# Kernel optimization log

Measured on AMD Instinct MI355X. Metric: run time of the kernel, lower is better.

The kernel has to match this reference:

```python
import jax, jax.numpy as jnp
import numpy as np


def _gcn_conv(x, W, b, row, col, norm, n_nodes):
    # x: [N, Fin]; W: [Fin, Fout]. PyG GCNConv: linear -> normalized gather/scatter-add -> +bias
    h = x @ W                                   # [N, Fout]
    msgs = h[row] * norm[:, None]               # [E+N, Fout] gather + scale
    out = jax.ops.segment_sum(msgs, col, num_segments=n_nodes)  # scatter-add
    return out + b


def _gcn_norm(edge_index, n_nodes):
    # add self-loops, then sym-normalize: deg^{-1/2}[row] * deg^{-1/2}[col]
    loops = jnp.arange(n_nodes, dtype=edge_index.dtype)
    row = jnp.concatenate([edge_index[0], loops])
    col = jnp.concatenate([edge_index[1], loops])
    ones = jnp.ones(row.shape[0], dtype=jnp.float32)
    deg = jax.ops.segment_sum(ones, col, num_segments=n_nodes)
    dinv = jnp.where(deg > 0, jax.lax.rsqrt(deg), 0.0)
    norm = dinv[row] * dinv[col]
    return row, col, norm


def setup_inputs() -> dict:
    key = jax.random.key(0)
    k1, k2, k3, k4 = jax.random.split(key, 4)
    N, E, F, H, C = 100000, 1600000, 256, 128, 40
    x = jax.random.normal(k1, (N, F), dtype=jnp.float32)
    edge_index = jax.random.randint(k2, (2, E), 0, N, dtype=jnp.int64)
    W1 = jax.random.normal(k3, (F, H), dtype=jnp.float32) * (1.0 / np.sqrt(F))
    b1 = jnp.zeros((H,), dtype=jnp.float32)
    W2 = jax.random.normal(k4, (H, C), dtype=jnp.float32) * (1.0 / np.sqrt(H))
    b2 = jnp.zeros((C,), dtype=jnp.float32)
    return {"x": x, "edge_index": edge_index, "W1": W1, "b1": b1, "W2": W2, "b2": b2}


def reference(x, edge_index, W1, b1, W2, b2):
    n_nodes = x.shape[0]
    row, col, norm = _gcn_norm(edge_index, n_nodes)
    h = _gcn_conv(x, W1, b1, row, col, norm, n_nodes)
    h = jax.nn.relu(h)
    # F.dropout in eval mode is identity (reference run deterministically)
    h = _gcn_conv(h, W2, b2, row, col, norm, n_nodes)
    return jax.nn.log_softmax(h, axis=1)
```

## Files before the change

### kernel.cpp

```cpp
#include <hip/hip_runtime.h>
#include <hip/hip_bf16.h>
#include <math.h>
#include <stdint.h>

typedef unsigned short u16;
typedef unsigned int u32;
typedef __attribute__((ext_vector_type(8))) short short8;
typedef __attribute__((ext_vector_type(4))) float f32x4;
typedef __attribute__((ext_vector_type(2))) float f32x2;

#define BN 256
#define NBMAX 400
#define EPB 4096
#define ST1 160
#define ST2 192

__device__ __forceinline__ u16 bfbits(float f) {
    __hip_bfloat16 h = __float2bfloat16(f);
    return *reinterpret_cast<u16*>(&h);
}
__device__ __forceinline__ float bflo(u32 v) { return __uint_as_float(v << 16); }
__device__ __forceinline__ float bfhi(u32 v) { return __uint_as_float(v & 0xffff0000u); }

template <bool HI>
__device__ __forceinline__ f32x2 fp8pair(u32 v) {
#if __has_builtin(__builtin_amdgcn_cvt_pk_f32_fp8)
    return __builtin_amdgcn_cvt_pk_f32_fp8(v, HI);
#else
    f32x2 r;
    r.x = __builtin_amdgcn_cvt_f32_fp8(v, HI ? 2 : 0);
    r.y = __builtin_amdgcn_cvt_f32_fp8(v, HI ? 3 : 1);
    return r;
#endif
}

__device__ __forceinline__ int sigma128(int col) {
    int a = col >> 6, c = (col >> 4) & 3, lr = col & 15;
    return (a << 6) + (lr << 2) + c;
}

__global__ __launch_bounds__(256) void k_pre(const int* __restrict__ ei, int E, int n, int nb,
                                             int nblkc, int* __restrict__ gcnt,
                                             const float* __restrict__ w1, short* __restrict__ w1bf,
                                             const float* __restrict__ b1, const float* __restrict__ w2,
                                             float* __restrict__ b1p, float* __restrict__ w2p) {
    __shared__ int sh[NBMAX];
    const int t = threadIdx.x;
    const int b = blockIdx.x;
    if (b < nblkc) {
        const int* col = ei + E;
        for (int i = t; i < nb; i += 256) sh[i] = 0;
        __syncthreads();
        const int base = b * EPB;
#pragma unroll
        for (int j = 0; j < 16; ++j) {
            int e = base + j * 256 + t;
            if (e < E) {
                unsigned c = (unsigned)col[e];
                if (c < (unsigned)n) atomicAdd(&sh[c >> 8], 1);
            }
        }
        __syncthreads();
        for (int i = t; i < nb; i += 256)
            if (sh[i]) atomicAdd(&gcnt[i], sh[i]);
    } else if (b < nblkc + 128) {
        int i = (b - nblkc) * 256 + t;
        int e = i & 7, l = (i >> 3) & 63, kt = (i >> 9) & 7, ct = i >> 12;
        int k = kt * 32 + (l >> 4) * 8 + e;
        int c = ct * 16 + (l & 15);
        w1bf[i] = (short)bfbits(w1[(size_t)k * 128 + c]);
    } else {
        int i = (b - nblkc - 128) * 256 + t;
        if (i < 128) b1p[sigma128(i)] = b1[i];
        int j = i - 128;
        if (j >= 0 && j < 128 * 40) {
            int col = j / 40, jj = j - col * 40;
            w2p[sigma128(col) * 40 + jj] = w2[j];
        }
    }
}

__global__ __launch_bounds__(512) void k_bscan(const int* __restrict__ gcnt,
                                               int* __restrict__ ebase, int* __restrict__ cursor,
                                               int* __restrict__ off, int nb, int n) {
    __shared__ int sh[512];
    const int t = threadIdx.x;
    int v = (t < nb) ? gcnt[t] : 0;
    sh[t] = v;
    __syncthreads();
    for (int d = 1; d < 512; d <<= 1) {
        int x = (t >= d) ? sh[t - d] : 0;
        __syncthreads();
        sh[t] += x;
        __syncthreads();
    }
    if (t < nb) {
        int excl = sh[t] - v;
        ebase[t] = excl;
        cursor[t] = excl;
    }
    if (t == 0) {
        ebase[nb] = sh[511];
        off[n] = sh[511] + n;
    }
}

__global__ __launch_bounds__(256) void k_scatg1(const int* __restrict__ ei,
                                                int* __restrict__ cursor, u32* __restrict__ staging,
                                                int E, int n, int nb, int nblks,
                                                const float* __restrict__ x,
                                                const short* __restrict__ w1bf,
                                                u32* __restrict__ hbf8) {
    __shared__ int cnt[NBMAX];
    __shared__ int cbase[NBMAX];
    const int t = threadIdx.x;
    if ((int)blockIdx.x < nblks) {
        for (int i = t; i < nb; i += 256) cnt[i] = 0;
        __syncthreads();
        const int base = blockIdx.x * EPB;
        int rr[16], cc[16], rk[16];
#pragma unroll
        for (int j = 0; j < 16; ++j) {
            int e = base + j * 256 + t;
            cc[j] = -1;
            if (e < E) {
                unsigned r = (unsigned)ei[e], c = (unsigned)ei[E + e];
                if (r < (unsigned)n && c < (unsigned)n) {
                    rr[j] = (int)r;
                    cc[j] = (int)c;
                    rk[j] = atomicAdd(&cnt[c >> 8], 1);
                }
            }
        }
        __syncthreads();
        for (int i = t; i < nb; i += 256)
            if (cnt[i]) cbase[i] = atomicAdd(&cursor[i], cnt[i]);
        __syncthreads();
#pragma unroll
        for (int j = 0; j < 16; ++j) {
            if (cc[j] >= 0) {
                int b = cc[j] >> 8;
                staging[cbase[b] + rk[j]] = (u32)rr[j] | ((u32)(cc[j] & (BN - 1)) << 17);
            }
        }
        return;
    }
    const int bid = blockIdx.x - nblks;
    const int wv = t >> 6, l = t & 63;
    const int mrow = wv >> 1, mcol = wv & 1;
    const int lr = l & 15, kg = l >> 4;
    const int n0 = bid * 64;

    const float* xp[2];
#pragma unroll
    for (int m = 0; m < 2; ++m) {
        int row = n0 + 32 * mrow + 16 * m + lr;
        if (row > n - 1) row = n - 1;
        xp[m] = x + (size_t)row * 256 + kg * 8;
    }
    const short* bbase = w1bf + ((size_t)(4 * mcol) * 8) * 64 * 8 + (size_t)l * 8;

    float4 xv[2][8][2];
#pragma unroll
    for (int kt = 0; kt < 8; ++kt)
#pragma unroll
        for (int m = 0; m < 2; ++m) {
            xv[m][kt][0] = *(const float4*)(xp[m] + kt * 32);
            xv[m][kt][1] = *(const float4*)(xp[m] + kt * 32 + 4);
        }

    f32x4 zero = {0.f, 0.f, 0.f, 0.f};
    f32x4 acc[2][4];
#pragma unroll
    for (int m = 0; m < 2; ++m)
#pragma unroll
        for (int c = 0; c < 4; ++c) acc[m][c] = zero;

#pragma unroll
    for (int kt = 0; kt < 8; ++kt) {
        short8 af[2];
#pragma unroll
        for (int m = 0; m < 2; ++m) {
            float4 u = xv[m][kt][0];
            float4 v = xv[m][kt][1];
            short8 a;
            a[0] = (short)bfbits(u.x);
            a[1] = (short)bfbits(u.y);
            a[2] = (short)bfbits(u.z);
            a[3] = (short)bfbits(u.w);
            a[4] = (short)bfbits(v.x);
            a[5] = (short)bfbits(v.y);
            a[6] = (short)bfbits(v.z);
            a[7] = (short)bfbits(v.w);
            af[m] = a;
        }
#pragma unroll
        for (int c = 0; c < 4; ++c) {
            short8 bfrag = *(const short8*)(bbase + ((size_t)(c * 8 + kt) * 64) * 8);
#pragma unroll
            for (int m = 0; m < 2; ++m)
                acc[m][c] = __builtin_amdgcn_mfma_f32_16x16x32_bf16(af[m], bfrag,
                                                                    acc[m][c], 0, 0, 0);
        }
    }

#pragma unroll
    for (int m = 0; m < 2; ++m) {
        int rbase = n0 + 32 * mrow + 16 * m + kg * 4;
#pragma unroll
        for (int r = 0; r < 4; ++r) {
            int row = rbase + r;
            if (row < n) {
                int w = __builtin_amdgcn_cvt_pk_fp8_f32(acc[m][0][r], acc[m][1][r], 0, false);
                w = __builtin_amdgcn_cvt_pk_fp8_f32(acc[m][2][r], acc[m][3][r], w, true);
                hbf8[(size_t)row * 32 + 16 * mcol + lr] = (u32)w;
            }
        }
    }
}

__global__ __launch_bounds__(256) void k_build(const u32* __restrict__ staging,
                                               const int* __restrict__ ebase,
                                               int* __restrict__ csrs, int* __restrict__ off,
                                               float* __restrict__ dinv, int n) {
    __shared__ int sh[256];
    __shared__ int cur[256];
    const int t = threadIdx.x;
    const int b = blockIdx.x;
    const int e0 = ebase[b], e1 = ebase[b + 1];
    const int node0 = b * BN;
    const int nn = min(BN, n - node0);
    sh[t] = 0;
    __syncthreads();
    for (int i = e0 + t; i < e1; i += 256)
        atomicAdd(&sh[staging[i] >> 17], 1);
    __syncthreads();
    const int mycnt = sh[t];
    const int myval = (t < nn) ? mycnt + 1 : 0;
    sh[t] = myval;
    __syncthreads();
    for (int d = 1; d < 256; d <<= 1) {
        int x = (t >= d) ? sh[t - d] : 0;
        __syncthreads();
        sh[t] += x;
        __syncthreads();
    }
    const int excl = sh[t] - myval;
    const int csrbase = e0 + node0;
    if (t < nn) {
        int node = node0 + t;
        int o = csrbase + excl;
        off[node] = o;
        dinv[node] = rsqrtf((float)(mycnt + 1));
        csrs[o] = node;
        cur[t] = o + 1;
    }
    __syncthreads();
    for (int i = e0 + t; i < e1; i += 256) {
        u32 v = staging[i];
        int p = atomicAdd(&cur[v >> 17], 1);
        csrs[p] = (int)(v & 0x1FFFF);
    }
}

__global__ __launch_bounds__(256) void k_agg1(const u32* __restrict__ hbf8,
                                              const int* __restrict__ off,
                                              const int* __restrict__ csrs,
                                              const float* __restrict__ dinv,
                                              const float* __restrict__ b1p,
                                              u16* __restrict__ h1b, int n) {
    __shared__ int s_s[8][ST1];
    __shared__ float s_f[8][ST1];
    const int t = threadIdx.x, h = t >> 5, fl = t & 31;
    const int node = blockIdx.x * 8 + h;
    const int nd = node < n ? node : n - 1;
    const float dn = dinv[nd];
    const int e0 = off[nd], e1 = off[nd + 1];
    const int deg = e1 - e0;
    const int nst = deg < ST1 ? deg : ST1;
    for (int i = fl; i < nst; i += 32) {
        int s = csrs[e0 + i];
        s_s[h][i] = s;
        s_f[h][i] = dinv[s] * dn;
    }
    __syncthreads();

    const int onst = __shfl_xor(nst, 32, 64);
    const int nmin = nst < onst ? nst : onst;
    const int nmax = nst > onst ? nst : onst;
    const int odeg = __shfl_xor(deg, 32, 64);
    const int dmax = deg > odeg ? deg : odeg;

    const u32* hb = hbf8;
    float a0 = 0.f, a1 = 0.f, a2 = 0.f, a3 = 0.f;
    int i = 0;
    for (; i + 16 <= nmin; i += 16) {
        u32 vv[16];
        float ww[16];
#pragma unroll
        for (int k = 0; k < 16; ++k) {
            int s = s_s[h][i + k];
            ww[k] = s_f[h][i + k];
            vv[k] = hb[(size_t)s * 32 + fl];
        }
#pragma unroll
        for (int k = 0; k < 16; ++k) {
            f32x2 lo = fp8pair<false>(vv[k]), hi = fp8pair<true>(vv[k]);
            a0 = fmaf(lo.x, ww[k], a0); a1 = fmaf(lo.y, ww[k], a1);
            a2 = fmaf(hi.x, ww[k], a2); a3 = fmaf(hi.y, ww[k], a3);
        }
    }
    for (; i + 4 <= nmin; i += 4) {
        u32 vv[4];
        float ww[4];
#pragma unroll
        for (int k = 0; k < 4; ++k) {
            int s = s_s[h][i + k];
            ww[k] = s_f[h][i + k];
            vv[k] = hb[(size_t)s * 32 + fl];
        }
#pragma unroll
        for (int k = 0; k < 4; ++k) {
            f32x2 lo = fp8pair<false>(vv[k]), hi = fp8pair<true>(vv[k]);
            a0 = fmaf(lo.x, ww[k], a0); a1 = fmaf(lo.y, ww[k], a1);
            a2 = fmaf(hi.x, ww[k], a2); a3 = fmaf(hi.y, ww[k], a3);
        }
    }
    for (; i < nmin; ++i) {
        int s = s_s[h][i];
        float w = s_f[h][i];
        u32 v = hb[(size_t)s * 32 + fl];
        f32x2 lo = fp8pair<false>(v), hi = fp8pair<true>(v);
        a0 = fmaf(lo.x, w, a0); a1 = fmaf(lo.y, w, a1);
        a2 = fmaf(hi.x, w, a2); a3 = fmaf(hi.y, w, a3);
    }
    for (; i < nmax; ++i) {
        bool ok = i < nst;
        int s = ok ? s_s[h][i] : nd;
        float w = ok ? s_f[h][i] : 0.f;
        u32 v = hb[(size_t)s * 32 + fl];
        f32x2 lo = fp8pair<false>(v), hi = fp8pair<true>(v);
        a0 = fmaf(lo.x, w, a0); a1 = fmaf(lo.y, w, a1);
        a2 = fmaf(hi.x, w, a2); a3 = fmaf(hi.y, w, a3);
    }
    for (int j = ST1; j < dmax; ++j) {
        bool ok = j < deg;
        int s = ok ? csrs[e0 + j] : nd;
        float w = ok ? dinv[s] * dn : 0.f;
        u32 v = hb[(size_t)s * 32 + fl];
        f32x2 lo = fp8pair<false>(v), hi = fp8pair<true>(v);
        a0 = fmaf(lo.x, w, a0); a1 = fmaf(lo.y, w, a1);
        a2 = fmaf(hi.x, w, a2); a3 = fmaf(hi.y, w, a3);
    }

    float4 bb = *(const float4*)(b1p + 4 * fl);
    float r0 = fmaxf(a0 + bb.x, 0.f);
    float r1 = fmaxf(a1 + bb.y, 0.f);
    float r2 = fmaxf(a2 + bb.z, 0.f);
    float r3 = fmaxf(a3 + bb.w, 0.f);
    if (node < n) {
        uint2 o;
        o.x = (u32)bfbits(r0) | ((u32)bfbits(r1) << 16);
        o.y = (u32)bfbits(r2) | ((u32)bfbits(r3) << 16);
        ((uint2*)h1b)[(size_t)node * 32 + fl] = o;
    }
}

__global__ __launch_bounds__(64) void k_gemm2(const u16* __restrict__ h1b,
                                              const float* __restrict__ w2p,
                                              u32* __restrict__ h2q, float* __restrict__ scl,
                                              int n) {
    __shared__ float hs[64 * 132];
    const int t = threadIdx.x;
    const int n0 = blockIdx.x * 64;
    const uint4* src = (const uint4*)(h1b + (size_t)n0 * 128);
#pragma unroll
    for (int i = 0; i < 16; ++i) {
        int idx = i * 64 + t;
        int r = idx >> 4, q = idx & 15;
        uint4 v = make_uint4(0u, 0u, 0u, 0u);
        if (n0 + r < n) v = src[(size_t)r * 16 + q];
        *(float4*)&hs[r * 132 + q * 8] =
            make_float4(bflo(v.x), bfhi(v.x), bflo(v.y), bfhi(v.y));
        *(float4*)&hs[r * 132 + q * 8 + 4] =
            make_float4(bflo(v.z), bfhi(v.z), bflo(v.w), bfhi(v.w));
    }
    __syncthreads();

    float acc[40];
#pragma unroll
    for (int c = 0; c < 40; ++c) acc[c] = 0.f;

    for (int k4 = 0; k4 < 32; ++k4) {
        float4 hv = *(const float4*)&hs[t * 132 + 4 * k4];
#pragma unroll
        for (int j = 0; j < 4; ++j) {
            float xv = (j == 0) ? hv.x : (j == 1) ? hv.y : (j == 2) ? hv.z : hv.w;
            const float* wr = w2p + (size_t)(4 * k4 + j) * 40;
#pragma unroll
            for (int c = 0; c < 40; ++c) acc[c] = fmaf(xv, wr[c], acc[c]);
        }
    }
    __syncthreads();

    float mx = 0.f;
#pragma unroll
    for (int c = 0; c < 40; ++c) mx = fmaxf(mx, fabsf(acc[c]));
    const float qs = mx > 0.f ? 127.f / mx : 0.f;
    u32* rowp = (u32*)hs + t * 16;
#pragma unroll
    for (int j = 0; j < 10; ++j) {
        u32 w = 0;
#pragma unroll
        for (int k = 0; k < 4; ++k) {
            int q = __float2int_rn(acc[4 * j + k] * qs);
            q = q > 127 ? 127 : (q < -127 ? -127 : q);
            w |= ((u32)(q & 255)) << (8 * k);
        }
        rowp[j] = w;
    }
#pragma unroll
    for (int j = 10; j < 16; ++j) rowp[j] = 0;
    __syncthreads();
    const int nrow = (n - n0 < 64) ? n - n0 : 64;
    uint4* dst = (uint4*)(h2q + (size_t)n0 * 16);
    const uint4* s4 = (const uint4*)hs;
#pragma unroll
    for (int i = 0; i < 4; ++i) {
        int idx = i * 64 + t;
        if ((idx >> 2) < nrow) dst[idx] = s4[idx];
    }
    if (t < nrow) scl[n0 + t] = mx * (1.f / 127.f);
}

__global__ __launch_bounds__(256) void k_agg2(const u32* __restrict__ h2q,
                                              const float* __restrict__ scl,
                                              const int* __restrict__ off,
                                              const int* __restrict__ csrs,
                                              const float* __restrict__ dinv,
                                              const float* __restrict__ b2,
                                              float* __restrict__ out, int n) {
    __shared__ int s_s[4][ST2];
    __shared__ float s_f[4][ST2];
    const int t = threadIdx.x, wv = t >> 6, l = t & 63;
    const int node = blockIdx.x * 4 + wv;
    const int nd = node < n ? node : n - 1;
    const float dn = dinv[nd];
    const int e0 = off[nd], e1 = off[nd + 1];
    const int deg = e1 - e0;
    const int nst = deg < ST2 ? deg : ST2;
    for (int i = l; i < nst; i += 64) {
        int s = csrs[e0 + i];
        s_s[wv][i] = s;
        s_f[wv][i] = dinv[s] * dn * scl[s];
    }
    __syncthreads();

    const int g = l >> 4;
    const int fl = l & 15;

#define ACC4(v, w)                                                         \
    {                                                                      \
        a0 = fmaf((float)(int)(signed char)((v) & 0xff), (w), a0);         \
        a1 = fmaf((float)(int)(signed char)(((v) >> 8) & 0xff), (w), a1);  \
        a2 = fmaf((float)(int)(signed char)(((v) >> 16) & 0xff), (w), a2); \
        a3 = fmaf((float)(int)(signed char)((v) >> 24), (w), a3);          \
    }

    float a0 = 0.f, a1 = 0.f, a2 = 0.f, a3 = 0.f;
    int base = 0;
    for (; base + 16 <= nst; base += 16) {
        int eA = base + g, eB = base + 4 + g, eC = base + 8 + g, eD = base + 12 + g;
        int sA = s_s[wv][eA], sB = s_s[wv][eB], sC = s_s[wv][eC], sD = s_s[wv][eD];
        float wA = s_f[wv][eA], wB = s_f[wv][eB], wC = s_f[wv][eC], wD = s_f[wv][eD];
        u32 vA = h2q[(size_t)sA * 16 + fl];
        u32 vB = h2q[(size_t)sB * 16 + fl];
        u32 vC = h2q[(size_t)sC * 16 + fl];
        u32 vD = h2q[(size_t)sD * 16 + fl];
        ACC4(vA, wA); ACC4(vB, wB); ACC4(vC, wC); ACC4(vD, wD);
    }
    for (; base < nst; base += 4) {
        int e = base + g;
        bool ok = e < nst;
        int s = ok ? s_s[wv][e] : nd;
        float w = ok ? s_f[wv][e] : 0.f;
        u32 v = h2q[(size_t)s * 16 + fl];
        ACC4(v, w);
    }
    for (int j = nst; j < deg; j += 4) {
        int e = j + g;
        bool ok = e < deg;
        int s = ok ? csrs[e0 + e] : nd;
        float w = ok ? dinv[s] * dn * scl[s] : 0.f;
        u32 v = h2q[(size_t)s * 16 + fl];
        ACC4(v, w);
    }
#undef ACC4

    float t0 = __shfl(a0, (l + 32) & 63, 64);
    float t1 = __shfl(a1, (l + 32) & 63, 64);
    float t2 = __shfl(a2, (l + 32) & 63, 64);
    float t3 = __shfl(a3, (l + 32) & 63, 64);
    a0 += t0; a1 += t1; a2 += t2; a3 += t3;
    t0 = __shfl(a0, (l + 16) & 63, 64);
    t1 = __shfl(a1, (l + 16) & 63, 64);
    t2 = __shfl(a2, (l + 16) & 63, 64);
    t3 = __shfl(a3, (l + 16) & 63, 64);
    a0 += t0; a1 += t1; a2 += t2; a3 += t3;

    const bool act = (l < 10);
    float4 bb = *(const float4*)(b2 + 4 * (act ? l : 9));
    float v0 = a0 + bb.x, v1 = a1 + bb.y, v2 = a2 + bb.z, v3 = a3 + bb.w;

    float m = act ? fmaxf(fmaxf(v0, v1), fmaxf(v2, v3)) : -INFINITY;
#pragma unroll
    for (int d = 8; d > 0; d >>= 1) m = fmaxf(m, __shfl_xor(m, d, 16));
    float s = act ? (__expf(v0 - m) + __expf(v1 - m) + __expf(v2 - m) + __expf(v3 - m)) : 0.f;
#pragma unroll
    for (int d = 8; d > 0; d >>= 1) s += __shfl_xor(s, d, 16);
    float ls = logf(s);
    if (node < n && act) {
        float4 o = make_float4(v0 - m - ls, v1 - m - ls, v2 - m - ls, v3 - m - ls);
        *(float4*)(out + (size_t)node * 40 + 4 * l) = o;
    }
}

extern "C" void kernel_launch(void* const* d_in, const int* in_sizes, int n_in,
                              void* d_out, int out_size, void* d_ws, size_t ws_size,
                              hipStream_t stream) {
    const float* x = (const float*)d_in[0];
    const int* ei = (const int*)d_in[1];
    const float* w1 = (const float*)d_in[2];
    const float* b1 = (const float*)d_in[3];
    const float* w2 = (const float*)d_in[4];
    const float* b2 = (const float*)d_in[5];
    float* out = (float*)d_out;

    const int N = in_sizes[0] / 256;
    const int E = in_sizes[1] / 2;
    const int NB = (N + BN - 1) / BN;

    char* p = (char*)d_ws;
    auto alloc = [&](size_t bytes) {
        char* r = p;
        p += (bytes + 255) & ~(size_t)255;
        return r;
    };
    int* gcnt = (int*)alloc((size_t)NB * 4);
    int* ebase = (int*)alloc((size_t)(NB + 1) * 4);
    int* cursor = (int*)alloc((size_t)NB * 4);
    int* off = (int*)alloc((size_t)(N + 1) * 4);
    float* dinv = (float*)alloc((size_t)N * 4);
    float* scl = (float*)alloc((size_t)N * 4);
    int* csrs = (int*)alloc((size_t)(E + N) * 4);
    short* w1bf = (short*)alloc(32768 * 2);
    float* b1p = (float*)alloc(128 * 4);
    float* w2p = (float*)alloc(128 * 40 * 4);
    u32* hbf8 = (u32*)alloc((size_t)N * 32 * 4);
    u16* h1b = (u16*)alloc((size_t)N * 128 * 2);
    u32* staging = (u32*)h1b;
    u32* h2q = hbf8;

    const int nblk = (E + EPB - 1) / EPB;
    const int g1blk = (N + 63) / 64;

    (void)hipMemsetAsync(gcnt, 0, (size_t)NB * 4, stream);
    k_pre<<<nblk + 128 + 21, 256, 0, stream>>>(ei, E, N, NB, nblk, gcnt, w1, w1bf,
                                               b1, w2, b1p, w2p);
    k_bscan<<<1, 512, 0, stream>>>(gcnt, ebase, cursor, off, NB, N);
    k_scatg1<<<nblk + g1blk, 256, 0, stream>>>(ei, cursor, staging, E, N, NB, nblk,
                                               x, w1bf, hbf8);
    k_build<<<NB, 256, 0, stream>>>(staging, ebase, csrs, off, dinv, N);
    k_agg1<<<(N + 7) / 8, 256, 0, stream>>>(hbf8, off, csrs, dinv, b1p, h1b, N);
    k_gemm2<<<g1blk, 64, 0, stream>>>(h1b, w2p, h2q, scl, N);
    k_agg2<<<(N + 3) / 4, 256, 0, stream>>>(h2q, scl, off, csrs, dinv, b2, out, N);
}
```

Baseline: 244.4 us.

## Stage x tile through swizzled LDS as bf16 before MFMA in fused GEMM

New measurement: 237.5 us (median of 2 runs). 2.8% less time.

```diff
diff --git a/kernel.cpp b/kernel.cpp
--- a/kernel.cpp
+++ b/kernel.cpp
@@ -105,17 +105,22 @@
     }
 }
 
+struct SMemScat { int cnt[NBMAX]; int cbase[NBMAX]; };
+union SMemU {
+    SMemScat s;
+    u16 xt[64 * 128];
+};
+
 __global__ __launch_bounds__(256) void k_scatg1(const int* __restrict__ ei,
                                                 int* __restrict__ cursor, u32* __restrict__ staging,
                                                 int E, int n, int nb, int nblks,
                                                 const float* __restrict__ x,
                                                 const short* __restrict__ w1bf,
                                                 u32* __restrict__ hbf8) {
-    __shared__ int cnt[NBMAX];
-    __shared__ int cbase[NBMAX];
+    __shared__ SMemU sm;
     const int t = threadIdx.x;
     if ((int)blockIdx.x < nblks) {
-        for (int i = t; i < nb; i += 256) cnt[i] = 0;
+        for (int i = t; i < nb; i += 256) sm.s.cnt[i] = 0;
         __syncthreads();
         const int base = blockIdx.x * EPB;
         int rr[16], cc[16], rk[16];
@@ -128,19 +133,19 @@
                 if (r < (unsigned)n && c < (unsigned)n) {
                     rr[j] = (int)r;
                     cc[j] = (int)c;
-                    rk[j] = atomicAdd(&cnt[c >> 8], 1);
+                    rk[j] = atomicAdd(&sm.s.cnt[c >> 8], 1);
                 }
             }
         }
         __syncthreads();
         for (int i = t; i < nb; i += 256)
-            if (cnt[i]) cbase[i] = atomicAdd(&cursor[i], cnt[i]);
+            if (sm.s.cnt[i]) sm.s.cbase[i] = atomicAdd(&cursor[i], sm.s.cnt[i]);
         __syncthreads();
 #pragma unroll
         for (int j = 0; j < 16; ++j) {
             if (cc[j] >= 0) {
                 int b = cc[j] >> 8;
-                staging[cbase[b] + rk[j]] = (u32)rr[j] | ((u32)(cc[j] & (BN - 1)) << 17);
+                staging[sm.s.cbase[b] + rk[j]] = (u32)rr[j] | ((u32)(cc[j] & (BN - 1)) << 17);
             }
         }
         return;
@@ -151,23 +156,7 @@
     const int lr = l & 15, kg = l >> 4;
     const int n0 = bid * 64;
 
-    const float* xp[2];
-#pragma unroll
-    for (int m = 0; m < 2; ++m) {
-        int row = n0 + 32 * mrow + 16 * m + lr;
-        if (row > n - 1) row = n - 1;
-        xp[m] = x + (size_t)row * 256 + kg * 8;
-    }
     const short* bbase = w1bf + ((size_t)(4 * mcol) * 8) * 64 * 8 + (size_t)l * 8;
-
-    float4 xv[2][8][2];
-#pragma unroll
-    for (int kt = 0; kt < 8; ++kt)
-#pragma unroll
-        for (int m = 0; m < 2; ++m) {
-            xv[m][kt][0] = *(const float4*)(xp[m] + kt * 32);
-            xv[m][kt][1] = *(const float4*)(xp[m] + kt * 32 + 4);
-        }
 
     f32x4 zero = {0.f, 0.f, 0.f, 0.f};
     f32x4 acc[2][4];
@@ -177,30 +166,42 @@
         for (int c = 0; c < 4; ++c) acc[m][c] = zero;
 
 #pragma unroll
-    for (int kt = 0; kt < 8; ++kt) {
-        short8 af[2];
-#pragma unroll
-        for (int m = 0; m < 2; ++m) {
-            float4 u = xv[m][kt][0];
-            float4 v = xv[m][kt][1];
-            short8 a;
-            a[0] = (short)bfbits(u.x);
-            a[1] = (short)bfbits(u.y);
-            a[2] = (short)bfbits(u.z);
-            a[3] = (short)bfbits(u.w);
-            a[4] = (short)bfbits(v.x);
-            a[5] = (short)bfbits(v.y);
-            a[6] = (short)bfbits(v.z);
-            a[7] = (short)bfbits(v.w);
-            af[m] = a;
-        }
-#pragma unroll
-        for (int c = 0; c < 4; ++c) {
-            short8 bfrag = *(const short8*)(bbase + ((size_t)(c * 8 + kt) * 64) * 8);
-#pragma unroll
-            for (int m = 0; m < 2; ++m)
-                acc[m][c] = __builtin_amdgcn_mfma_f32_16x16x32_bf16(af[m], bfrag,
-                                                                    acc[m][c], 0, 0, 0);
+    for (int p = 0; p < 2; ++p) {
+        __syncthreads();
+#pragma unroll
+        for (int j = 0; j < 8; ++j) {
+            int idx = j * 256 + t;
+            int row = idx >> 5;
+            int kf4 = idx & 31;
+            int grow = n0 + row;
+            if (grow > n - 1) grow = n - 1;
+            float4 v = *(const float4*)(x + (size_t)grow * 256 + p * 128 + kf4 * 4);
+            u32 w0 = (u32)bfbits(v.x) | ((u32)bfbits(v.y) << 16);
+            u32 w1v = (u32)bfbits(v.z) | ((u32)bfbits(v.w) << 16);
+            int bir = kf4 * 8;
+            int sb = row * 256 + (bir ^ ((row & 7) << 4));
+            *(uint2*)((char*)sm.xt + sb) = make_uint2(w0, w1v);
+        }
+        __syncthreads();
+#pragma unroll
+        for (int ktl = 0; ktl < 4; ++ktl) {
+            int kt = p * 4 + ktl;
+            short8 af[2];
+#pragma unroll
+            for (int m = 0; m < 2; ++m) {
+                int r = 32 * mrow + 16 * m + lr;
+                int bir = ktl * 64 + kg * 16;
+                int sb = r * 256 + (bir ^ ((r & 7) << 4));
+                af[m] = *(const short8*)((const char*)sm.xt + sb);
+            }
+#pragma unroll
+            for (int c = 0; c < 4; ++c) {
+                short8 bfrag = *(const short8*)(bbase + ((size_t)(c * 8 + kt) * 64) * 8);
+#pragma unroll
+                for (int m = 0; m < 2; ++m)
+                    acc[m][c] = __builtin_amdgcn_mfma_f32_16x16x32_bf16(af[m], bfrag,
+                                                                        acc[m][c], 0, 0, 0);
+            }
         }
     }
 
```
